# Performance work log

Hardware: AMD Instinct MI355X
Metric: run time of the kernel (lower is better)

The kernel has to match this reference:

```python
import jax, jax.numpy as jnp
import numpy as np

RADII = (0.8, 1.6)
NSAMPLES = (16, 32)
IN_C = 64
BN_EPS = 1e-3  # BN1d eps; eval-mode BN with running stats (0, 1)
B, N_PER, M_PER = 2, 8192, 2048
BOX = (40.0, 40.0, 4.0)  # point cloud extent in meters


def _batch_ids(cnt, total):
    # point i belongs to batch searchsorted(cumsum(cnt), i, 'right')
    return jnp.searchsorted(jnp.cumsum(cnt), jnp.arange(total), side='right')


def _ball_group(xyz, bid, new_xyz, nbid, feats, radius, nsample):
    # Ball query (stacked-batch): first `nsample` points within `radius` of each
    # query, same batch only; pad short balls with the first found index;
    # fully-empty balls are zeroed (pcdet QueryAndGroup semantics).
    d2 = jnp.sum((new_xyz[:, None, :] - xyz[None, :, :]) ** 2, axis=-1)  # (M, N)
    within = (d2 < radius * radius) & (nbid[:, None] == bid[None, :])
    n = xyz.shape[0]
    score = jnp.where(within, -jnp.arange(n, dtype=jnp.float32), -jnp.inf)
    vals, idx = jax.lax.top_k(score, nsample)  # smallest in-ball indices first
    valid = jnp.isfinite(vals)
    idx = jnp.where(valid, idx, idx[:, :1])  # pad with first found index
    empty = ~valid[:, :1]  # (M, 1): no point in ball
    g_xyz = xyz[idx] - new_xyz[:, None, :]          # (M, ns, 3) relative coords
    g = jnp.concatenate([g_xyz, feats[idx]], -1)    # (M, ns, 3 + C), xyz first
    return jnp.where(empty[:, :, None], 0.0, g)


def _shared_mlp(x, layers):
    # Conv1d(k=1, bias=False) + BN1d(eval, mean=0, var=1) + ReLU per layer
    inv_std = 1.0 / jnp.sqrt(1.0 + BN_EPS)
    for w, g, b in layers:
        x = jnp.einsum('mnc,oc->mno', x, w)
        x = jax.nn.relu(x * (g * inv_std) + b)
    return x  # (M, ns, cout)


def setup_inputs() -> dict:
    key = jax.random.key(0)
    ks = jax.random.split(key, 16)
    box = jnp.asarray(BOX, dtype=jnp.float32)
    xyz = jax.random.uniform(ks[0], (B * N_PER, 3), dtype=jnp.float32) * box
    new_xyz = jax.random.uniform(ks[1], (B * M_PER, 3), dtype=jnp.float32) * box
    features = jax.random.normal(ks[2], (B * N_PER, IN_C), dtype=jnp.float32)

    def conv_w(k, cin, cout):
        return jax.random.normal(k, (cout, cin), dtype=jnp.float32) / np.sqrt(cin)

    cin = IN_C + 3  # use_xyz -> +3
    inp = dict(xyz=xyz, features=features, new_xyz=new_xyz,
               w00=conv_w(ks[3], cin, 64), g00=jnp.ones(64), b00=jnp.zeros(64),
               w01=conv_w(ks[4], 64, 64), g01=jnp.ones(64), b01=jnp.zeros(64),
               w10=conv_w(ks[5], cin, 64), g10=jnp.ones(64), b10=jnp.zeros(64),
               w11=conv_w(ks[6], 64, 64), g11=jnp.ones(64), b11=jnp.zeros(64),
               xyz_batch_cnt=jnp.full((B,), N_PER, dtype=jnp.int32),
               new_xyz_batch_cnt=jnp.full((B,), M_PER, dtype=jnp.int32))
    return inp


def reference(xyz, features, new_xyz,
              w00, g00, b00, w01, g01, b01,
              w10, g10, b10, w11, g11, b11,
              xyz_batch_cnt, new_xyz_batch_cnt):
    bid = _batch_ids(xyz_batch_cnt, xyz.shape[0])
    nbid = _batch_ids(new_xyz_batch_cnt, new_xyz.shape[0])
    layer_params = [[(w00, g00, b00), (w01, g01, b01)],
                    [(w10, g10, b10), (w11, g11, b11)]]
    outs = []
    for k in range(len(RADII)):
        g = _ball_group(xyz, bid, new_xyz, nbid, features, RADII[k], NSAMPLES[k])
        h = _shared_mlp(g, layer_params[k])
        outs.append(jnp.max(h, axis=1))  # max-pool over neighbors
    return jnp.concatenate(outs, axis=1)  # (M_tot, 128)
```

## Files before the change

### kernel.cpp

```cpp
#include <hip/hip_runtime.h>
#include <hip/hip_bf16.h>
#include <stdint.h>


#define NS0 16
#define NS1 32
#define NXC 25
#define NYC 25
#define NZC 3
#define CPB (NXC * NYC * NZC)
#define CINV 0.625f
#define CSZ 1.6f
#define CAP 48

typedef _Float16 half8 __attribute__((ext_vector_type(8)));
typedef float f32x4 __attribute__((ext_vector_type(4)));

static __device__ __forceinline__ half8 cvt8(float4 a, float4 b) {
    half8 r;
    r[0] = (_Float16)a.x; r[1] = (_Float16)a.y; r[2] = (_Float16)a.z; r[3] = (_Float16)a.w;
    r[4] = (_Float16)b.x; r[5] = (_Float16)b.y; r[6] = (_Float16)b.z; r[7] = (_Float16)b.w;
    return r;
}
static __device__ __forceinline__ uint32_t pk2(float x, float y) {
    const _Float16 a = (_Float16)x, c = (_Float16)y;
    return (uint32_t)__builtin_bit_cast(uint16_t, a) |
           ((uint32_t)__builtin_bit_cast(uint16_t, c) << 16);
}

__global__ __launch_bounds__(256) void prep(
    const float* __restrict__ w00, const float* __restrict__ g00, const float* __restrict__ b00,
    const float* __restrict__ w01, const float* __restrict__ g01, const float* __restrict__ b01,
    const float* __restrict__ w10, const float* __restrict__ g10, const float* __restrict__ b10,
    const float* __restrict__ w11, const float* __restrict__ g11, const float* __restrict__ b11,
    float* __restrict__ wpk, int* __restrict__ cell_cnt, int n4)
{
    if (blockIdx.x >= 2) {
        const int i = (blockIdx.x - 2) * 256 + threadIdx.x;
        if (i < n4) ((int4*)cell_cnt)[i] = make_int4(0, 0, 0, 0);
        return;
    }
    const int k = blockIdx.x;
    const int tid = threadIdx.x;
    const int lane = tid & 63, t = tid >> 6;
    const int p = lane & 15, h = lane >> 4;
    const float* W1 = k ? w10 : w00; const float* G1 = k ? g10 : g00; const float* B1 = k ? b10 : b00;
    const float* W2 = k ? w11 : w01; const float* G2 = k ? g11 : g01; const float* B2 = k ? b11 : b01;
    const float inv = 1.0f / sqrtf(1.0f + 1e-3f);

    uint32_t* outw = (uint32_t*)wpk + (size_t)k * 6144;
    const int m = 16 * t + p;
    const float sc1 = G1[m] * inv;
    #pragma unroll
    for (int s = 0; s < 3; ++s) {
        #pragma unroll
        for (int r = 0; r < 4; ++r) {
            uint32_t u = 0;
            #pragma unroll
            for (int e = 0; e < 2; ++e) {
                const int cpad = 32 * s + 8 * h + 2 * r + e;
                float val = 0.f;
                if (cpad < 64)       val = W1[m * 67 + 3 + cpad] * sc1;
                else if (cpad < 67)  val = W1[m * 67 + (cpad - 64)] * sc1;
                else if (cpad == 67) val = B1[m];
                const _Float16 hv = (_Float16)val;
                u |= ((uint32_t)__builtin_bit_cast(uint16_t, hv)) << (16 * e);
            }
            outw[((t * 3 + s) * 64 + lane) * 4 + r] = u;
        }
    }
    const float sc2 = G2[m] * inv;
    uint32_t* outw2 = outw + 3072;
    #pragma unroll
    for (int s = 0; s < 2; ++s) {
        #pragma unroll
        for (int r = 0; r < 4; ++r) {
            uint32_t u = 0;
            #pragma unroll
            for (int e = 0; e < 2; ++e) {
                const int cch = 32 * s + 8 * h + 2 * r + e;
                const _Float16 hv = (_Float16)(W2[m * 64 + cch] * sc2);
                u |= ((uint32_t)__builtin_bit_cast(uint16_t, hv)) << (16 * e);
            }
            outw2[((t * 2 + s) * 64 + lane) * 4 + r] = u;
        }
    }
    float* bo = wpk + (size_t)k * 6144 + 5120;
    #pragma unroll
    for (int r = 0; r < 4; ++r)
        bo[(t * 64 + lane) * 4 + r] = B2[16 * t + 4 * h + r];
}

__global__ __launch_bounds__(256) void bin_cap(
    const float* __restrict__ xyz, const int* __restrict__ xcnt, int B, int N,
    int* __restrict__ cell_cnt, float4* __restrict__ binned4)
{
    const int i = blockIdx.x * 256 + threadIdx.x;
    if (i >= N) return;
    int acc = 0, b = 0;
    for (int k = 0; k < B; ++k) { int c = xcnt[k]; if (i >= acc && i < acc + c) b = k; acc += c; }
    const float x = xyz[3 * i], y = xyz[3 * i + 1], z = xyz[3 * i + 2];
    const int cx = min(NXC - 1, max(0, (int)floorf(x * CINV)));
    const int cy = min(NYC - 1, max(0, (int)floorf(y * CINV)));
    const int cz = min(NZC - 1, max(0, (int)floorf(z * CINV)));
    const int cell = b * CPB + (cz * NYC + cy) * NXC + cx;
    const int slot = atomicAdd(&cell_cnt[cell], 1);
    if (slot < CAP) {
        float4 r; r.x = x; r.y = y; r.z = z; r.w = __int_as_float(i);
        binned4[(size_t)cell * CAP + slot] = r;
    }
}

static __device__ __forceinline__ void mlp_one(
    int c_pts, int ntmax, const int* __restrict__ L,
    float qx, float qy, float qz,
    const uint4* __restrict__ wlds, char* __restrict__ hb,
    const float* __restrict__ xyz, const float* __restrict__ feats,
    const float4* __restrict__ bq, float* __restrict__ out_base,
    bool qvalid, int lane)
{
    const int p = lane & 15, h = lane >> 4;
    const int nt = min((c_pts + 15) >> 4, ntmax);

    f32x4 macc[4] = {f32x4(-3e38f), f32x4(-3e38f), f32x4(-3e38f), f32x4(-3e38f)};

    half8 b0a[2], b1a[2], b2a[2];
    bool ona[2];
    #pragma unroll
    for (int pt = 0; pt < 2; ++pt) {
        b0a[pt] = 0; b1a[pt] = 0; b2a[pt] = 0; ona[pt] = false;
        if (pt < nt) {
            const int gp = pt * 16 + p;
            const bool on = gp < c_pts;
            ona[pt] = on;
            if (on) {
                const int j = L[gp];
                const float4* f0p = (const float4*)(feats + (size_t)j * 64 + 8 * h);
                const float4* f1p = (const float4*)(feats + (size_t)j * 64 + 32 + 8 * h);
                b0a[pt] = cvt8(f0p[0], f0p[1]);
                b1a[pt] = cvt8(f1p[0], f1p[1]);
                if (h == 0) {
                    half8 b2 = 0;
                    b2[0] = (_Float16)(xyz[3 * j + 0] - qx);
                    b2[1] = (_Float16)(xyz[3 * j + 1] - qy);
                    b2[2] = (_Float16)(xyz[3 * j + 2] - qz);
                    b2[3] = (_Float16)1.0f;
                    b2a[pt] = b2;
                }
            }
        }
    }

    #pragma unroll
    for (int pt = 0; pt < 2; ++pt) {
        if (pt < nt) {
            f32x4 acc[4] = {f32x4(0.f), f32x4(0.f), f32x4(0.f), f32x4(0.f)};
            #pragma unroll
            for (int t = 0; t < 4; ++t) {
                #pragma unroll
                for (int s = 0; s < 3; ++s) {
                    const half8 a = __builtin_bit_cast(half8, wlds[(t * 3 + s) * 64 + lane]);
                    const half8 bf = (s == 0) ? b0a[pt] : ((s == 1) ? b1a[pt] : b2a[pt]);
                    acc[t] = __builtin_amdgcn_mfma_f32_16x16x32_f16(a, bf, acc[t], 0, 0, 0);
                }
            }
            #pragma unroll
            for (int t = 0; t < 4; ++t) {
                *(uint32_t*)(hb + 144 * p + 32 * t + 8 * h) =
                    pk2(fmaxf(acc[t][0], 0.f), fmaxf(acc[t][1], 0.f));
                *(uint32_t*)(hb + 144 * p + 32 * t + 8 * h + 4) =
                    pk2(fmaxf(acc[t][2], 0.f), fmaxf(acc[t][3], 0.f));
            }
            const half8 g0 = *(const half8*)(hb + 144 * p + 16 * h);
            const half8 g1 = *(const half8*)(hb + 144 * p + 64 + 16 * h);

            f32x4 acc2[4] = {f32x4(0.f), f32x4(0.f), f32x4(0.f), f32x4(0.f)};
            #pragma unroll
            for (int t = 0; t < 4; ++t) {
                #pragma unroll
                for (int s = 0; s < 2; ++s) {
                    const half8 a = __builtin_bit_cast(half8, wlds[768 + (t * 2 + s) * 64 + lane]);
                    const half8 bf = (s == 0) ? g0 : g1;
                    acc2[t] = __builtin_amdgcn_mfma_f32_16x16x32_f16(a, bf, acc2[t], 0, 0, 0);
                }
            }
            #pragma unroll
            for (int t = 0; t < 4; ++t)
                #pragma unroll
                for (int r = 0; r < 4; ++r)
                    if (ona[pt]) macc[t][r] = fmaxf(macc[t][r], acc2[t][r]);
        }
    }

    #pragma unroll
    for (int d = 1; d < 16; d <<= 1)
        #pragma unroll
        for (int t = 0; t < 4; ++t)
            #pragma unroll
            for (int r = 0; r < 4; ++r)
                macc[t][r] = fmaxf(macc[t][r], __shfl_xor(macc[t][r], d));

    if (p == 0 && qvalid) {
        float* o = out_base + 4 * h;
        #pragma unroll
        for (int t = 0; t < 4; ++t) {
            const float4 bb = bq[t * 64 + lane];
            float4 v;
            v.x = fmaxf(macc[t][0] + bb.x, 0.f);
            v.y = fmaxf(macc[t][1] + bb.y, 0.f);
            v.z = fmaxf(macc[t][2] + bb.z, 0.f);
            v.w = fmaxf(macc[t][3] + bb.w, 0.f);
            *(float4*)(o + 16 * t) = v;
        }
    }
}

__global__ __launch_bounds__(256) void query_mlp(
    const float* __restrict__ xyz, const float* __restrict__ feats,
    const float* __restrict__ new_xyz, const int* __restrict__ ncnt,
    const int* __restrict__ cell_cnt, const float4* __restrict__ binned4,
    const float* __restrict__ wpk, int B, int M,
    float* __restrict__ out)
{
    __shared__ uint4 wlds[1280];
    __shared__ uint32_t cand[4][128];
    __shared__ int lidx[4][NS0 + NS1];
    __shared__ uint4 hbuf[4][144];

    const int tid = threadIdx.x;
    const int wave = tid >> 6, lane = tid & 63;
    const int gw = blockIdx.x * 4 + wave;
    const bool qvalid = gw < M;
    const int m = qvalid ? gw : 0;

    {
        const uint4* ws = (const uint4*)((const uint32_t*)wpk);
        #pragma unroll
        for (int i = 0; i < 5; ++i) wlds[tid + 256 * i] = ws[tid + 256 * i];
    }

    int cA = 0, cB = 0;
    float qx, qy, qz;
    {
        int acc = 0, b = 0;
        for (int k2 = 0; k2 < B; ++k2) { int c = ncnt[k2]; if (m >= acc && m < acc + c) b = k2; acc += c; }
        qx = new_xyz[3 * m]; qy = new_xyz[3 * m + 1]; qz = new_xyz[3 * m + 2];
        const float R0S = 0.64f, R1S = 2.56f;
        const float PAD = 1.60002f;

        const int lx = max(0, (int)floorf((qx - PAD) * CINV));
        const int hx = min(NXC - 1, (int)floorf((qx + PAD) * CINV));
        const int ly = max(0, (int)floorf((qy - PAD) * CINV));
        const int hy = min(NYC - 1, (int)floorf((qy + PAD) * CINV));
        const int lz = max(0, (int)floorf((qz - PAD) * CINV));
        const int hz = min(NZC - 1, (int)floorf((qz + PAD) * CINV));
        const int wx = hx - lx + 1, wy = hy - ly + 1, wz = hz - lz + 1;
        const int nw = wx * wy * wz;

        int cnt_l = 0, cell_l = 0;
        if (lane < nw) {
            const int wxy = wx * wy;
            const int ldz = lane / wxy;
            const int rem = lane - ldz * wxy;
            const int ldy = rem / wx;
            const int ldx = rem - ldy * wx;
            const int cx = lx + ldx, cy = ly + ldy, cz = lz + ldz;
            const float bx0 = cx * CSZ, by0 = cy * CSZ, bz0 = cz * CSZ;
            const float dx = (qx < bx0) ? (bx0 - qx) : ((qx > bx0 + CSZ) ? (qx - bx0 - CSZ) : 0.f);
            const float dy = (qy < by0) ? (by0 - qy) : ((qy > by0 + CSZ) ? (qy - by0 - CSZ) : 0.f);
            const float dz = (qz < bz0) ? (bz0 - qz) : ((qz > bz0 + CSZ) ? (qz - bz0 - CSZ) : 0.f);
            const float md2 = dx * dx + dy * dy + dz * dz;
            cell_l = b * CPB + (cz * NYC + cy) * NXC + cx;
            if (md2 <= R1S + 1e-3f) cnt_l = min(cell_cnt[cell_l], CAP);
        }

        int incl = cnt_l;
        #pragma unroll
        for (int d = 1; d < 64; d <<= 1) {
            const int v = __shfl_up(incl, d);
            if (lane >= d) incl += v;
        }
        const int excl = incl - cnt_l;
        const int tot = __shfl(incl, 63);

        uint32_t* cd = cand[wave];
        const unsigned long long lower = (lane == 0) ? 0ull : (~0ull >> (64 - lane));
        int c = 0, c0n = 0;

        for (int t0 = 0; t0 < tot; t0 += 64) {
            const int t = t0 + lane;
            const bool v = t < tot;
            int lo = 0, hi = 63;
            #pragma unroll
            for (int s = 0; s < 6; ++s) {
                const int mid = (lo + hi) >> 1;
                const int vm = __shfl(incl, mid);
                if (vm > t) hi = mid; else lo = mid + 1;
            }
            const int j = lo & 63;
            const int slot = t - __shfl(excl, j);
            const int cell = __shfl(cell_l, j);
            float d2 = 1e30f;
            int pid = 0;
            if (v) {
                const float4 e = binned4[(size_t)cell * CAP + slot];
                pid = __float_as_int(e.w);
                const float dx = e.x - qx, dy = e.y - qy, dzp = e.z - qz;
                d2 = __fadd_rn(__fadd_rn(__fmul_rn(dx, dx), __fmul_rn(dy, dy)),
                               __fmul_rn(dzp, dzp));
            }
            const bool keep = v && (d2 < R1S);
            const bool f0 = keep && (d2 < R0S);
            const unsigned long long mk = __ballot(keep);
            if (keep) {
                const int pos = c + __popcll(mk & lower);
                if (pos < 128) cd[pos] = ((uint32_t)pid << 1) | (f0 ? 1u : 0u);
            }
            c += __popcll(mk);
            c0n += __popcll(__ballot(f0));
        }

        const int cc = min(c, 128);
        int* L = &lidx[wave][0];
        const uint32_t ka = (lane < cc) ? cd[lane] : 0xFFFFFFFFu;
        const uint32_t kb = (64 + lane < cc) ? cd[64 + lane] : 0xFFFFFFFFu;
        int ra = 0, ra0 = 0, rb = 0, rb0 = 0;
        for (int e2 = 0; e2 < cc; e2 += 4) {
            #pragma unroll
            for (int u = 0; u < 4; ++u) {
                const int ee = e2 + u;
                if (ee < cc) {
                    const uint32_t ke = cd[ee];
                    const int sm_a = (ke < ka), sm_b = (ke < kb), f = (int)(ke & 1u);
                    ra += sm_a; ra0 += sm_a & f;
                    rb += sm_b; rb0 += sm_b & f;
                }
            }
        }
        if (lane < cc) {
            const int pid = (int)(ka >> 1);
            if ((ka & 1u) && ra0 < NS0) L[ra0] = pid;
            if (ra < NS1) L[NS0 + ra] = pid;
        }
        if (64 + lane < cc) {
            const int pid = (int)(kb >> 1);
            if ((kb & 1u) && rb0 < NS0) L[rb0] = pid;
            if (rb < NS1) L[NS0 + rb] = pid;
        }
        cA = min(c0n, NS0);
        cB = min(c, NS1);
    }

    __syncthreads();

    char* hb = (char*)&hbuf[wave][0];
    mlp_one(cA, 1, &lidx[wave][0], qx, qy, qz, wlds, hb, xyz, feats,
            (const float4*)(wpk + 5120), out + (size_t)m * 128, qvalid, lane);

    __syncthreads();

    {
        const uint4* ws = (const uint4*)((const uint32_t*)wpk + 6144);
        #pragma unroll
        for (int i = 0; i < 5; ++i) wlds[tid + 256 * i] = ws[tid + 256 * i];
    }
    __syncthreads();

    mlp_one(cB, 2, &lidx[wave][NS0], qx, qy, qz, wlds, hb, xyz, feats,
            (const float4*)(wpk + 6144 + 5120), out + (size_t)m * 128 + 64,
            qvalid, lane);
}

extern "C" void kernel_launch(void* const* d_in, const int* in_sizes, int n_in,
                              void* d_out, int out_size, void* d_ws, size_t ws_size,
                              hipStream_t stream) {
    const float* xyz     = (const float*)d_in[0];
    const float* feats   = (const float*)d_in[1];
    const float* new_xyz = (const float*)d_in[2];
    const float* w00 = (const float*)d_in[3];
    const float* g00 = (const float*)d_in[4];
    const float* b00 = (const float*)d_in[5];
    const float* w01 = (const float*)d_in[6];
    const float* g01 = (const float*)d_in[7];
    const float* b01 = (const float*)d_in[8];
    const float* w10 = (const float*)d_in[9];
    const float* g10 = (const float*)d_in[10];
    const float* b10 = (const float*)d_in[11];
    const float* w11 = (const float*)d_in[12];
    const float* g11 = (const float*)d_in[13];
    const float* b11 = (const float*)d_in[14];
    const int* xcnt = (const int*)d_in[15];
    const int* ncnt = (const int*)d_in[16];

    const int B = in_sizes[15];
    const int N = in_sizes[0] / 3;
    const int M = in_sizes[2] / 3;
    const int ncells = B * CPB;
    const int ncells_pad = (ncells + 3) & ~3;

    uint32_t* w32 = (uint32_t*)d_ws;
    float* wpk      = (float*)w32;
    int* cell_cnt   = (int*)(w32 + 12288);
    float4* binned4 = (float4*)(cell_cnt + ncells_pad);

    const int n4 = ncells_pad >> 2;
    const int zero_blocks = (n4 + 255) / 256;
    prep<<<2 + zero_blocks, 256, 0, stream>>>(
        w00, g00, b00, w01, g01, b01, w10, g10, b10, w11, g11, b11,
        wpk, cell_cnt, n4);
    bin_cap<<<(N + 255) / 256, 256, 0, stream>>>(xyz, xcnt, B, N,
                                                 cell_cnt, binned4);
    query_mlp<<<(M + 3) / 4, 256, 0, stream>>>(xyz, feats, new_xyz, ncnt,
                                               cell_cnt, binned4, wpk, B, M,
                                               (float*)d_out);
}
```

Measured before the change: 33.53 us.

## Split the two radius scales into separate blocks to double grid parallelism

```diff
diff --git a/kernel.cpp b/kernel.cpp
--- a/kernel.cpp
+++ b/kernel.cpp
@@ -219,34 +219,35 @@
     const float* __restrict__ xyz, const float* __restrict__ feats,
     const float* __restrict__ new_xyz, const int* __restrict__ ncnt,
     const int* __restrict__ cell_cnt, const float4* __restrict__ binned4,
-    const float* __restrict__ wpk, int B, int M,
+    const float* __restrict__ wpk, int B, int M, int MB4,
     float* __restrict__ out)
 {
     __shared__ uint4 wlds[1280];
     __shared__ uint32_t cand[4][128];
-    __shared__ int lidx[4][NS0 + NS1];
+    __shared__ int lidx[4][NS1];
     __shared__ uint4 hbuf[4][144];
 
     const int tid = threadIdx.x;
     const int wave = tid >> 6, lane = tid & 63;
-    const int gw = blockIdx.x * 4 + wave;
-    const bool qvalid = gw < M;
-    const int m = qvalid ? gw : 0;
+    const int kblk = (blockIdx.x >= (unsigned)MB4) ? 1 : 0;
+    const int q = (blockIdx.x - kblk * MB4) * 4 + wave;
+    const bool qvalid = q < M;
+    const int m = qvalid ? q : 0;
 
     {
-        const uint4* ws = (const uint4*)((const uint32_t*)wpk);
+        const uint4* ws = (const uint4*)((const uint32_t*)wpk + (size_t)kblk * 6144);
         #pragma unroll
         for (int i = 0; i < 5; ++i) wlds[tid + 256 * i] = ws[tid + 256 * i];
     }
 
-    int cA = 0, cB = 0;
+    int cnt = 0;
     float qx, qy, qz;
     {
         int acc = 0, b = 0;
         for (int k2 = 0; k2 < B; ++k2) { int c = ncnt[k2]; if (m >= acc && m < acc + c) b = k2; acc += c; }
         qx = new_xyz[3 * m]; qy = new_xyz[3 * m + 1]; qz = new_xyz[3 * m + 2];
-        const float R0S = 0.64f, R1S = 2.56f;
-        const float PAD = 1.60002f;
+        const float RS = kblk ? 2.56f : 0.64f;
+        const float PAD = kblk ? 1.60002f : 0.80002f;
 
         const int lx = max(0, (int)floorf((qx - PAD) * CINV));
         const int hx = min(NXC - 1, (int)floorf((qx + PAD) * CINV));
@@ -271,7 +272,7 @@
             const float dz = (qz < bz0) ? (bz0 - qz) : ((qz > bz0 + CSZ) ? (qz - bz0 - CSZ) : 0.f);
             const float md2 = dx * dx + dy * dy + dz * dz;
             cell_l = b * CPB + (cz * NYC + cy) * NXC + cx;
-            if (md2 <= R1S + 1e-3f) cnt_l = min(cell_cnt[cell_l], CAP);
+            if (md2 <= RS + 1e-3f) cnt_l = min(cell_cnt[cell_l], CAP);
         }
 
         int incl = cnt_l;
@@ -285,7 +286,7 @@
 
         uint32_t* cd = cand[wave];
         const unsigned long long lower = (lane == 0) ? 0ull : (~0ull >> (64 - lane));
-        int c = 0, c0n = 0;
+        int c = 0;
 
         for (int t0 = 0; t0 < tot; t0 += 64) {
             const int t = t0 + lane;
@@ -309,66 +310,47 @@
                 d2 = __fadd_rn(__fadd_rn(__fmul_rn(dx, dx), __fmul_rn(dy, dy)),
                                __fmul_rn(dzp, dzp));
             }
-            const bool keep = v && (d2 < R1S);
-            const bool f0 = keep && (d2 < R0S);
+            const bool keep = v && (d2 < RS);
             const unsigned long long mk = __ballot(keep);
             if (keep) {
                 const int pos = c + __popcll(mk & lower);
-                if (pos < 128) cd[pos] = ((uint32_t)pid << 1) | (f0 ? 1u : 0u);
+                if (pos < 128) cd[pos] = (uint32_t)pid;
             }
             c += __popcll(mk);
-            c0n += __popcll(__ballot(f0));
-        }
-
+        }
+
+        const int NSk = kblk ? NS1 : NS0;
         const int cc = min(c, 128);
         int* L = &lidx[wave][0];
         const uint32_t ka = (lane < cc) ? cd[lane] : 0xFFFFFFFFu;
         const uint32_t kb = (64 + lane < cc) ? cd[64 + lane] : 0xFFFFFFFFu;
-        int ra = 0, ra0 = 0, rb = 0, rb0 = 0;
+        int ra = 0, rb = 0;
         for (int e2 = 0; e2 < cc; e2 += 4) {
             #pragma unroll
             for (int u = 0; u < 4; ++u) {
                 const int ee = e2 + u;
                 if (ee < cc) {
                     const uint32_t ke = cd[ee];
-                    const int sm_a = (ke < ka), sm_b = (ke < kb), f = (int)(ke & 1u);
-                    ra += sm_a; ra0 += sm_a & f;
-                    rb += sm_b; rb0 += sm_b & f;
+                    ra += (ke < ka);
+                    rb += (ke < kb);
                 }
             }
         }
-        if (lane < cc) {
-            const int pid = (int)(ka >> 1);
-            if ((ka & 1u) && ra0 < NS0) L[ra0] = pid;
-            if (ra < NS1) L[NS0 + ra] = pid;
-        }
-        if (64 + lane < cc) {
-            const int pid = (int)(kb >> 1);
-            if ((kb & 1u) && rb0 < NS0) L[rb0] = pid;
-            if (rb < NS1) L[NS0 + rb] = pid;
-        }
-        cA = min(c0n, NS0);
-        cB = min(c, NS1);
+        if (lane < cc && ra < NSk) L[ra] = (int)ka;
+        if (64 + lane < cc && rb < NSk) L[rb] = (int)kb;
+        cnt = min(c, NSk);
     }
 
     __syncthreads();
 
     char* hb = (char*)&hbuf[wave][0];
-    mlp_one(cA, 1, &lidx[wave][0], qx, qy, qz, wlds, hb, xyz, feats,
-            (const float4*)(wpk + 5120), out + (size_t)m * 128, qvalid, lane);
-
-    __syncthreads();
-
-    {
-        const uint4* ws = (const uint4*)((const uint32_t*)wpk + 6144);
-        #pragma unroll
-        for (int i = 0; i < 5; ++i) wlds[tid + 256 * i] = ws[tid + 256 * i];
-    }
-    __syncthreads();
-
-    mlp_one(cB, 2, &lidx[wave][NS0], qx, qy, qz, wlds, hb, xyz, feats,
-            (const float4*)(wpk + 6144 + 5120), out + (size_t)m * 128 + 64,
-            qvalid, lane);
+    if (!kblk)
+        mlp_one(cnt, 1, &lidx[wave][0], qx, qy, qz, wlds, hb, xyz, feats,
+                (const float4*)(wpk + 5120), out + (size_t)m * 128, qvalid, lane);
+    else
+        mlp_one(cnt, 2, &lidx[wave][0], qx, qy, qz, wlds, hb, xyz, feats,
+                (const float4*)(wpk + 6144 + 5120), out + (size_t)m * 128 + 64,
+                qvalid, lane);
 }
 
 extern "C" void kernel_launch(void* const* d_in, const int* in_sizes, int n_in,
@@ -410,7 +392,8 @@
         wpk, cell_cnt, n4);
     bin_cap<<<(N + 255) / 256, 256, 0, stream>>>(xyz, xcnt, B, N,
                                                  cell_cnt, binned4);
-    query_mlp<<<(M + 3) / 4, 256, 0, stream>>>(xyz, feats, new_xyz, ncnt,
-                                               cell_cnt, binned4, wpk, B, M,
-                                               (float*)d_out);
-}
+    const int MB4 = (M + 3) / 4;
+    query_mlp<<<2 * MB4, 256, 0, stream>>>(xyz, feats, new_xyz, ncnt,
+                                           cell_cnt, binned4, wpk, B, M, MB4,
+                                           (float*)d_out);
+}
```

Result: slower. 36.26 us (+8.2%).
